# Kernel optimization log

Measured on AMD Instinct MI355X. Metric: run time of the kernel, lower is better.

## Reference

```python
import jax, jax.numpy as jnp
import numpy as np

N_NODES = 20000
N_EDGES = 160000
F_IN = 128
H1 = 1024  # 128 * out_channels
H2 = 512   # 64 * out_channels
OUT = 8    # out_channels


def graph_conv(x, src, dst, w_rel, b_rel, w_root):
    # PyG GraphConv(aggr='mean'): out = lin_rel(mean_{j->i} x_j) + lin_root(x_i)
    n = x.shape[0]
    agg = jax.ops.segment_sum(x[src], dst, num_segments=n)          # [N, F_in]
    deg = jax.ops.segment_sum(jnp.ones((src.shape[0],), x.dtype), dst, num_segments=n)
    mean = agg / jnp.maximum(deg, 1.0)[:, None]
    return mean @ w_rel + b_rel + x @ w_root


def setup_inputs() -> dict:
    key = jax.random.key(0)
    ks = jax.random.split(key, 12)
    x = jax.random.normal(ks[0], (N_NODES, F_IN), dtype=jnp.float32)
    edge_index = jax.random.randint(ks[1], (2, N_EDGES), 0, N_NODES, dtype=jnp.int64)

    def lin(k, fi, fo):
        return jax.random.normal(k, (fi, fo), dtype=jnp.float32) / np.sqrt(fi)

    return {
        "x": x,
        "edge_index": edge_index,
        "w1_rel": lin(ks[2], F_IN, H1), "b1": jnp.zeros((H1,), jnp.float32), "w1_root": lin(ks[3], F_IN, H1),
        "w2_rel": lin(ks[4], H1, H2), "b2": jnp.zeros((H2,), jnp.float32), "w2_root": lin(ks[5], H1, H2),
        "wmu_rel": lin(ks[6], H2, OUT), "bmu": jnp.zeros((OUT,), jnp.float32), "wmu_root": lin(ks[7], H2, OUT),
        "wls_rel": lin(ks[8], H2, OUT), "bls": jnp.zeros((OUT,), jnp.float32), "wls_root": lin(ks[9], H2, OUT),
    }


def reference(x, edge_index, w1_rel, b1, w1_root, w2_rel, b2, w2_root,
              wmu_rel, bmu, wmu_root, wls_rel, bls, wls_root):
    src, dst = edge_index[0], edge_index[1]
    h = jax.nn.relu(graph_conv(x, src, dst, w1_rel, b1, w1_root))
    h = jax.nn.relu(graph_conv(h, src, dst, w2_rel, b2, w2_root))
    mu = graph_conv(h, src, dst, wmu_rel, bmu, wmu_root)
    logstd = graph_conv(h, src, dst, wls_rel, bls, wls_root)
    return (mu, logstd)
```

## Files before the change

### kernel.cpp

```cpp
#include <hip/hip_runtime.h>

typedef __attribute__((ext_vector_type(8))) short short8;
typedef __attribute__((ext_vector_type(4))) float f32x4;
typedef unsigned long long u64;

__device__ __forceinline__ unsigned short f2bf(float f) {
  union { float f; unsigned u; } v; v.f = f;
  unsigned u = v.u;
  unsigned r = (u + 0x7FFFu + ((u >> 16) & 1u)) >> 16;
  return (unsigned short)r;
}
__device__ __forceinline__ float bf2f(unsigned short s) {
  union { unsigned u; float f; } v; v.u = ((unsigned)s) << 16;
  return v.f;
}

__device__ __forceinline__ void gl_lds16(const unsigned short* g, unsigned short* l) {
  __builtin_amdgcn_global_load_lds(
      (const __attribute__((address_space(1))) void*)g,
      (__attribute__((address_space(3))) void*)l, 16, 0, 0);
}

__device__ __forceinline__ int detect64(const void* edges, int n_nodes) {
  const long long* p = (const long long*)edges;
  int ok = 1;
#pragma unroll
  for (int i = 0; i < 8; ++i) {
    long long v = p[i];
    if (v < 0 || v >= n_nodes) ok = 0;
  }
  return ok;
}


__device__ __forceinline__ void ttile(const float* __restrict__ src, int Nw,
                                      unsigned short* __restrict__ dst, int ldd,
                                      int rowoff, int coloff,
                                      int tileIdx, int tilesN, float (*tile)[33]) {
  int tk = tileIdx / tilesN, tn = tileIdx % tilesN;
  int k0 = tk * 32, n0 = tn * 32;
  int tx = threadIdx.x & 31, ty = threadIdx.x >> 5;
#pragma unroll
  for (int s = 0; s < 4; ++s)
    tile[ty + s * 8][tx] = src[(size_t)(k0 + ty + s * 8) * Nw + n0 + tx];
  __syncthreads();
#pragma unroll
  for (int s = 0; s < 4; ++s)
    dst[(size_t)(rowoff + n0 + ty + s * 8) * ldd + coloff + k0 + tx] =
        f2bf(tile[tx][ty + s * 8]);
}

__global__ void prep_kernel(int* deg, int* cursor, int n,
                            const float* __restrict__ x, unsigned short* __restrict__ xb,
                            int total4,
                            const float* __restrict__ w1_rel, const float* __restrict__ w1_root,
                            const float* __restrict__ w2_rel, const float* __restrict__ w2_root,
                            const float* __restrict__ wmu_rel, const float* __restrict__ wmu_root,
                            const float* __restrict__ wls_rel, const float* __restrict__ wls_root,
                            unsigned short* __restrict__ Bt1,
                            unsigned short* __restrict__ Bt2,
                            unsigned short* __restrict__ Bt3) {
  __shared__ float tile[32][33];
  int b = blockIdx.x;
  if (b >= 1408) {
    int b4 = (b - 1408) * 1024;
#pragma unroll
    for (int s = 0; s < 4; ++s) {
      int i4 = b4 + s * 256 + threadIdx.x;
      if (i4 < total4) {
        float4 v = reinterpret_cast<const float4*>(x)[i4];
        ushort4 o;
        o.x = f2bf(v.x); o.y = f2bf(v.y); o.z = f2bf(v.z); o.w = f2bf(v.w);
        reinterpret_cast<ushort4*>(xb)[i4] = o;
      }
    }
    return;
  }
  if (b >= 1344) {
    int i = (b - 1344) * blockDim.x + threadIdx.x;
    int stride = 64 * blockDim.x;
    for (int j = i; j < n; j += stride) { deg[j] = 0; cursor[j] = 0; }
    return;
  }
  if (b < 128)       ttile(w1_rel, 1024, Bt1, 256, 0, 0, b, 32, tile);
  else if (b < 256)  ttile(w1_root, 1024, Bt1, 256, 0, 128, b - 128, 32, tile);
  else if (b < 768)  ttile(w2_rel, 512, Bt2, 1024, 0, 0, b - 256, 16, tile);
  else if (b < 1280) ttile(w2_root, 512, Bt2, 1024, 512, 0, b - 768, 16, tile);
  else {
    int idx = (b - 1280) * 256 + threadIdx.x;
    int nn = idx >> 9, k = idx & 511;
    float v;
    if (nn < 8) v = wmu_rel[(size_t)k * 8 + nn];
    else if (nn < 16) v = wmu_root[(size_t)k * 8 + (nn - 8)];
    else if (nn < 24) v = wls_rel[(size_t)k * 8 + (nn - 16)];
    else v = wls_root[(size_t)k * 8 + (nn - 24)];
    Bt3[(size_t)nn * 512 + k] = f2bf(v);
  }
}

__device__ __forceinline__ int edge_at(const void* p, int is64, size_t idx) {
  return is64 ? (int)((const long long*)p)[idx] : ((const int*)p)[idx];
}

__global__ void count_kernel(const void* edges, int E, int n_nodes, int* deg) {
  int is64 = detect64(edges, n_nodes);
  int i = blockIdx.x * blockDim.x + threadIdx.x;
  int stride = gridDim.x * blockDim.x;
  for (int e = i; e < E; e += stride) {
    int d = edge_at(edges, is64, (size_t)E + e);
    atomicAdd(&deg[d], 1);
  }
}

__global__ void scan_kernel(const int* __restrict__ deg, int* __restrict__ rs,
                            float* __restrict__ invdeg, int n) {
  __shared__ int ssum[1024];
  int tid = threadIdx.x;
  int chunk = (n + 1023) >> 10;
  int start = tid * chunk;
  int end = min(start + chunk, n);
  int s = 0;
  for (int i = start; i < end; ++i) s += deg[i];
  ssum[tid] = s;
  __syncthreads();
  for (int off = 1; off < 1024; off <<= 1) {
    int t = (tid >= off) ? ssum[tid - off] : 0;
    __syncthreads();
    ssum[tid] += t;
    __syncthreads();
  }
  int run = (tid ? ssum[tid - 1] : 0);
  if (tid == 0) rs[0] = 0;
  for (int i = start; i < end; ++i) {
    int d = deg[i];
    run += d;
    rs[i + 1] = run;
    invdeg[i] = 1.0f / fmaxf((float)d, 1.0f);
  }
}

__global__ void fill_kernel(const void* edges, int E, int n_nodes,
                            const int* __restrict__ rs, int* cursor, int* col_src) {
  int is64 = detect64(edges, n_nodes);
  int i = blockIdx.x * blockDim.x + threadIdx.x;
  int stride = gridDim.x * blockDim.x;
  for (int e = i; e < E; e += stride) {
    int d = edge_at(edges, is64, (size_t)E + e);
    int s = edge_at(edges, is64, (size_t)e);
    int p = atomicAdd(&cursor[d], 1);
    col_src[rs[d] + p] = s;
  }
}


__global__ void agg1_kernel(const unsigned short* __restrict__ xb,
                            const int* __restrict__ rs, const int* __restrict__ cs,
                            const float* __restrict__ invdeg,
                            unsigned short* __restrict__ A1, int M) {
  int node = blockIdx.x * 4 + (threadIdx.x >> 6);
  if (node >= M) return;
  int c0 = (threadIdx.x & 63) * 2;
  float a0 = 0.f, a1 = 0.f;
  int e1 = rs[node + 1];
  for (int e = rs[node]; e < e1; ++e) {
    unsigned w = *reinterpret_cast<const unsigned*>(xb + (size_t)cs[e] * 128 + c0);
    a0 += bf2f((unsigned short)(w & 0xffff));
    a1 += bf2f((unsigned short)(w >> 16));
  }
  float inv = invdeg[node];
  unsigned root = *reinterpret_cast<const unsigned*>(xb + (size_t)node * 128 + c0);
  unsigned mean = (unsigned)f2bf(a0 * inv) | ((unsigned)f2bf(a1 * inv) << 16);
  *reinterpret_cast<unsigned*>(A1 + (size_t)node * 256 + c0) = mean;
  *reinterpret_cast<unsigned*>(A1 + (size_t)node * 256 + 128 + c0) = root;
}

__global__ void agg2_kernel(const unsigned short* __restrict__ P2,
                            const int* __restrict__ rs, const int* __restrict__ cs,
                            const float* __restrict__ invdeg,
                            const float* __restrict__ b2,
                            unsigned short* __restrict__ h2, int M) {
  int node = blockIdx.x * 4 + (threadIdx.x >> 6);
  if (node >= M) return;
  int f0 = (threadIdx.x & 63) * 8;
  float acc[8];
#pragma unroll
  for (int v = 0; v < 8; ++v) acc[v] = 0.f;
  int e1 = rs[node + 1];
  for (int e = rs[node]; e < e1; ++e) {
    int s = cs[e];
    uint4 w = *reinterpret_cast<const uint4*>(P2 + (size_t)s * 1024 + f0);
    acc[0] += bf2f((unsigned short)(w.x & 0xffff));
    acc[1] += bf2f((unsigned short)(w.x >> 16));
    acc[2] += bf2f((unsigned short)(w.y & 0xffff));
    acc[3] += bf2f((unsigned short)(w.y >> 16));
    acc[4] += bf2f((unsigned short)(w.z & 0xffff));
    acc[5] += bf2f((unsigned short)(w.z >> 16));
    acc[6] += bf2f((unsigned short)(w.w & 0xffff));
    acc[7] += bf2f((unsigned short)(w.w >> 16));
  }
  float inv = invdeg[node];
  uint4 wr = *reinterpret_cast<const uint4*>(P2 + (size_t)node * 1024 + 512 + f0);
  float rt[8] = {
    bf2f((unsigned short)(wr.x & 0xffff)), bf2f((unsigned short)(wr.x >> 16)),
    bf2f((unsigned short)(wr.y & 0xffff)), bf2f((unsigned short)(wr.y >> 16)),
    bf2f((unsigned short)(wr.z & 0xffff)), bf2f((unsigned short)(wr.z >> 16)),
    bf2f((unsigned short)(wr.w & 0xffff)), bf2f((unsigned short)(wr.w >> 16))};
  unsigned short o[8];
#pragma unroll
  for (int v = 0; v < 8; ++v)
    o[v] = f2bf(fmaxf(acc[v] * inv + rt[v] + b2[f0 + v], 0.f));
  uint4 pk;
  pk.x = (unsigned)o[0] | ((unsigned)o[1] << 16);
  pk.y = (unsigned)o[2] | ((unsigned)o[3] << 16);
  pk.z = (unsigned)o[4] | ((unsigned)o[5] << 16);
  pk.w = (unsigned)o[6] | ((unsigned)o[7] << 16);
  *reinterpret_cast<uint4*>(h2 + (size_t)node * 512 + f0) = pk;
}

__global__ void head_agg_kernel(const float* __restrict__ P3,
                                const int* __restrict__ rs, const int* __restrict__ cs,
                                const float* __restrict__ invdeg,
                                const float* __restrict__ bmu, const float* __restrict__ bls,
                                float* __restrict__ outmu, float* __restrict__ outls, int M) {
  int idx = blockIdx.x * blockDim.x + threadIdx.x;
  int node = idx >> 4;
  int c = idx & 15;
  if (node >= M) return;
  int relc = (c < 8) ? c : (16 + (c - 8));
  float acc = 0.f;
  int e1 = rs[node + 1];
  for (int e = rs[node]; e < e1; ++e) acc += P3[(size_t)cs[e] * 32 + relc];
  float v = acc * invdeg[node] + P3[(size_t)node * 32 + relc + 8]
          + ((c < 8) ? bmu[c] : bls[c - 8]);
  if (c < 8) outmu[(size_t)node * 8 + c] = v;
  else outls[(size_t)node * 8 + (c - 8)] = v;
}

__launch_bounds__(256, 4)
__global__ void gemm_db_kernel(const unsigned short* __restrict__ A, int lda,
                               const unsigned short* __restrict__ Bt, int ldb,
                               const float* __restrict__ bias,
                               void* __restrict__ outp, int ldo,
                               int M, int N, int K, int relu, int out_f32, int gx) {
  __shared__ unsigned short As[2 * 4096];
  __shared__ unsigned short Bs[2 * 4096];
  const int tid = threadIdx.x;
  const int lane = tid & 63;
  const int w = tid >> 6;
  const int wr = w >> 1, wc = w & 1;
  const int lr = lane & 15, lk = lane >> 4;
  const int sw8 = (lk ^ ((lr >> 1) & 3)) * 8;

  int nwg = gridDim.x, orig = blockIdx.x;
  int q = nwg >> 3, r = nwg & 7;
  int xcd = orig & 7, lid = orig >> 3;
  int swz = (xcd < r ? xcd * (q + 1) : r * (q + 1) + (xcd - r) * q) + lid;
  int m0 = (swz / gx) * 128, n0 = (swz % gx) * 128;

  f32x4 acc[4][4];
#pragma unroll
  for (int i = 0; i < 4; ++i)
#pragma unroll
    for (int j = 0; j < 4; ++j) acc[i][j] = (f32x4)0.0f;

  const int r0 = tid >> 2;
  const int slog = ((tid & 3) ^ ((r0 >> 1) & 3)) * 8;
  const unsigned short* gA = A + (size_t)(m0 + r0) * lda + slog;
  const unsigned short* gB = Bt + (size_t)(n0 + r0) * ldb + slog;
  const size_t a64 = (size_t)64 * lda, b64 = (size_t)64 * ldb;
  unsigned short* wa = As + w * 512;
  unsigned short* wb = Bs + w * 512;

  auto STG = [&](int s, int t) {
    const unsigned short* a = gA + (size_t)t * 32;
    const unsigned short* b = gB + (size_t)t * 32;
    gl_lds16(a, wa + s * 4096);
    gl_lds16(a + a64, wa + s * 4096 + 2048);
    gl_lds16(b, wb + s * 4096);
    gl_lds16(b + b64, wb + s * 4096 + 2048);
  };

  const int nt = K >> 5;
  STG(0, 0);
  __syncthreads();

  int buf = 0;
  for (int t = 0; t < nt; ++t) {
    if (t + 1 < nt) STG(buf ^ 1, t + 1);
    const unsigned short* as_ = As + buf * 4096;
    const unsigned short* bs_ = Bs + buf * 4096;
    short8 af[4], bf[4];
#pragma unroll
    for (int i = 0; i < 4; ++i) {
      af[i] = *reinterpret_cast<const short8*>(&as_[(wr * 64 + i * 16 + lr) * 32 + sw8]);
      bf[i] = *reinterpret_cast<const short8*>(&bs_[(wc * 64 + i * 16 + lr) * 32 + sw8]);
    }
    __builtin_amdgcn_s_setprio(1);
#pragma unroll
    for (int i = 0; i < 4; ++i)
#pragma unroll
      for (int j = 0; j < 4; ++j)
        acc[i][j] = __builtin_amdgcn_mfma_f32_16x16x32_bf16(af[i], bf[j], acc[i][j], 0, 0, 0);
    __builtin_amdgcn_s_setprio(0);
    if (t + 1 < nt) __syncthreads();
    buf ^= 1;
  }

#pragma unroll
  for (int i = 0; i < 4; ++i) {
    int row_b = m0 + wr * 64 + i * 16 + lk * 4;
#pragma unroll
    for (int j = 0; j < 4; ++j) {
      int col = n0 + wc * 64 + j * 16 + lr;
      float bv = bias ? bias[col] : 0.f;
#pragma unroll
      for (int rr = 0; rr < 4; ++rr) {
        int row = row_b + rr;
        if (row < M) {
          float v = acc[i][j][rr] + bv;
          if (relu) v = fmaxf(v, 0.f);
          if (out_f32) ((float*)outp)[(size_t)row * ldo + col] = v;
          else ((unsigned short*)outp)[(size_t)row * ldo + col] = f2bf(v);
        }
      }
    }
  }
}

__launch_bounds__(256, 3)
__global__ void gemm_heads_kernel(const unsigned short* __restrict__ A,
                                  const unsigned short* __restrict__ Bt3,
                                  float* __restrict__ P3, int M) {
  __shared__ unsigned short Bs[16 * 1024];
  __shared__ unsigned short As[2 * 4096];
  const int tid = threadIdx.x;
  const int lane = tid & 63;
  const int w = tid >> 6;
  const int lr = lane & 15, lk = lane >> 4;
  const int sw8 = (lk ^ ((lr >> 1) & 3)) * 8;

  int nwg = gridDim.x, orig = blockIdx.x;
  int q = nwg >> 3, r = nwg & 7;
  int xcd = orig & 7, lid = orig >> 3;
  int swz = (xcd < r ? xcd * (q + 1) : r * (q + 1) + (xcd - r) * q) + lid;
  int m0 = swz * 128;

  for (int i = 0; i < 8; ++i) {
    int j = i * 256 + tid;
    int n = j >> 6, p = j & 63;
    int x = (n >> 1) & 3;
    uint4 v = *reinterpret_cast<const uint4*>(Bt3 + (size_t)n * 512 + ((p & ~3) | ((p & 3) ^ x)) * 8);
    *reinterpret_cast<uint4*>(&Bs[(p >> 2) * 1024 + n * 32 + (p & 3) * 8]) = v;
  }

  f32x4 acc[2][2];
#pragma unroll
  for (int i = 0; i < 2; ++i)
#pragma unroll
    for (int j = 0; j < 2; ++j) acc[i][j] = (f32x4)0.0f;

  const int r0 = tid >> 2;
  const int slog = ((tid & 3) ^ ((r0 >> 1) & 3)) * 8;
  const unsigned short* gA = A + (size_t)(m0 + r0) * 512 + slog;
  const size_t a64 = (size_t)64 * 512;
  unsigned short* wa = As + w * 512;

  auto STG = [&](int s, int t) {
    const unsigned short* a = gA + (size_t)t * 32;
    gl_lds16(a, wa + s * 4096);
    gl_lds16(a + a64, wa + s * 4096 + 2048);
  };

  STG(0, 0);
  __syncthreads();

  int buf = 0;
  const int nt = 16;
  for (int t = 0; t < nt; ++t) {
    if (t + 1 < nt) STG(buf ^ 1, t + 1);
    const unsigned short* as_ = As + buf * 4096;
    short8 af[2], bf[2];
#pragma unroll
    for (int i = 0; i < 2; ++i) {
      af[i] = *reinterpret_cast<const short8*>(&as_[(w * 32 + i * 16 + lr) * 32 + sw8]);
      bf[i] = *reinterpret_cast<const short8*>(&Bs[t * 1024 + (i * 16 + lr) * 32 + sw8]);
    }
#pragma unroll
    for (int i = 0; i < 2; ++i)
#pragma unroll
      for (int j = 0; j < 2; ++j)
        acc[i][j] = __builtin_amdgcn_mfma_f32_16x16x32_bf16(af[i], bf[j], acc[i][j], 0, 0, 0);
    if (t + 1 < nt) __syncthreads();
    buf ^= 1;
  }

#pragma unroll
  for (int i = 0; i < 2; ++i) {
    int row_b = m0 + w * 32 + i * 16 + lk * 4;
#pragma unroll
    for (int j = 0; j < 2; ++j) {
      int col = j * 16 + lr;
#pragma unroll
      for (int rr = 0; rr < 4; ++rr) {
        int row = row_b + rr;
        if (row < M) P3[(size_t)row * 32 + col] = acc[i][j][rr];
      }
    }
  }
}


extern "C" void kernel_launch(void* const* d_in, const int* in_sizes, int n_in,
                              void* d_out, int out_size, void* d_ws, size_t ws_size,
                              hipStream_t stream) {
  const float* x = (const float*)d_in[0];
  const void* edge = d_in[1];
  const float* w1_rel = (const float*)d_in[2];
  const float* b1 = (const float*)d_in[3];
  const float* w1_root = (const float*)d_in[4];
  const float* w2_rel = (const float*)d_in[5];
  const float* b2 = (const float*)d_in[6];
  const float* w2_root = (const float*)d_in[7];
  const float* wmu_rel = (const float*)d_in[8];
  const float* bmu = (const float*)d_in[9];
  const float* wmu_root = (const float*)d_in[10];
  const float* wls_rel = (const float*)d_in[11];
  const float* bls = (const float*)d_in[12];
  const float* wls_root = (const float*)d_in[13];

  const int FIN = 128, H1 = 1024, H2 = 512;
  const int M = in_sizes[0] / FIN;
  const int E = in_sizes[1] / 2;
  const int Mpad = ((M + 127) / 128) * 128;
  const int gy = Mpad / 128;

  char* ws = (char*)d_ws;
  size_t off = 0;
  auto alloc = [&](size_t bytes) -> char* {
    char* p = ws + off;
    off = (off + bytes + 255) & ~(size_t)255;
    return p;
  };
  int* deg = (int*)alloc((size_t)M * 4);
  int* cursor = (int*)alloc((size_t)M * 4);
  int* rs = (int*)alloc((size_t)(M + 1) * 4);
  float* invdeg = (float*)alloc((size_t)M * 4);
  int* cs = (int*)alloc((size_t)E * 4);
  unsigned short* xb = (unsigned short*)alloc((size_t)M * 128 * 2);
  unsigned short* A1 = (unsigned short*)alloc((size_t)Mpad * 256 * 2);
  unsigned short* h1 = (unsigned short*)alloc((size_t)Mpad * 1024 * 2);
  unsigned short* P2 = (unsigned short*)alloc((size_t)Mpad * 1024 * 2);
  unsigned short* h2 = (unsigned short*)alloc((size_t)Mpad * 512 * 2);
  float* P3 = (float*)alloc((size_t)Mpad * 32 * 4);
  unsigned short* Bt1 = (unsigned short*)alloc((size_t)H1 * 256 * 2);
  unsigned short* Bt2 = (unsigned short*)alloc((size_t)1024 * 1024 * 2);
  unsigned short* Bt3 = (unsigned short*)alloc((size_t)32 * 512 * 2);

  prep_kernel<<<2048, 256, 0, stream>>>(deg, cursor, M,
                                        x, xb, M * FIN / 4,
                                        w1_rel, w1_root, w2_rel, w2_root,
                                        wmu_rel, wmu_root, wls_rel, wls_root,
                                        Bt1, Bt2, Bt3);
  count_kernel<<<256, 256, 0, stream>>>(edge, E, M, deg);
  scan_kernel<<<1, 1024, 0, stream>>>(deg, rs, invdeg, M);
  fill_kernel<<<256, 256, 0, stream>>>(edge, E, M, rs, cursor, cs);

  agg1_kernel<<<(M + 3) / 4, 256, 0, stream>>>(xb, rs, cs, invdeg, A1, M);
  gemm_db_kernel<<<(H1 / 128) * gy, 256, 0, stream>>>(
      A1, 256, Bt1, 256, b1, h1, 1024, M, H1, 256, 1, 0, H1 / 128);

  gemm_db_kernel<<<(1024 / 128) * gy, 256, 0, stream>>>(
      h1, 1024, Bt2, 1024, nullptr, P2, 1024, M, 1024, 1024, 0, 0, 1024 / 128);
  agg2_kernel<<<(M + 3) / 4, 256, 0, stream>>>(P2, rs, cs, invdeg, b2, h2, M);

  gemm_heads_kernel<<<gy, 256, 0, stream>>>(h2, Bt3, P3, M);
  float* outmu = (float*)d_out;
  float* outls = outmu + (size_t)M * 8;
  head_agg_kernel<<<(M * 16 + 255) / 256, 256, 0, stream>>>(
      P3, rs, cs, invdeg, bmu, bls, outmu, outls, M);
}
```

Measured before the change: 236.8 us.

## Fuse CSR build into one cooperative kernel with grid-wide syncs

Replaces the separate count, single-block scan and fill kernels, plus the degree/cursor zeroing in prep, with one cooperative kernel of 512 blocks that uses grid.sync between phases. The scan becomes a multi-block scan: each block scans locally and then sums earlier block totals read from a small buffer. This removes several kernel launches and spreads the serial 1024-thread scan across the whole GPU. It adds four grid-wide barriers and relies on all 512 blocks being co-resident for the cooperative launch.

```diff
diff --git a/kernel.cpp b/kernel.cpp
--- a/kernel.cpp
+++ b/kernel.cpp
@@ -1,4 +1,7 @@
 #include <hip/hip_runtime.h>
+#include <hip/hip_cooperative_groups.h>
+
+namespace cg = cooperative_groups;
 
 typedef __attribute__((ext_vector_type(8))) short short8;
 typedef __attribute__((ext_vector_type(4))) float f32x4;
@@ -30,6 +33,10 @@
     if (v < 0 || v >= n_nodes) ok = 0;
   }
   return ok;
+}
+
+__device__ __forceinline__ int edge_at(const void* p, int is64, size_t idx) {
+  return is64 ? (int)((const long long*)p)[idx] : ((const int*)p)[idx];
 }
 
 
@@ -50,8 +57,7 @@
         f2bf(tile[tx][ty + s * 8]);
 }
 
-__global__ void prep_kernel(int* deg, int* cursor, int n,
-                            const float* __restrict__ x, unsigned short* __restrict__ xb,
+__global__ void prep_kernel(const float* __restrict__ x, unsigned short* __restrict__ xb,
                             int total4,
                             const float* __restrict__ w1_rel, const float* __restrict__ w1_root,
                             const float* __restrict__ w2_rel, const float* __restrict__ w2_root,
@@ -62,8 +68,8 @@
                             unsigned short* __restrict__ Bt3) {
   __shared__ float tile[32][33];
   int b = blockIdx.x;
-  if (b >= 1408) {
-    int b4 = (b - 1408) * 1024;
+  if (b >= 1344) {
+    int b4 = (b - 1344) * 1024;
 #pragma unroll
     for (int s = 0; s < 4; ++s) {
       int i4 = b4 + s * 256 + threadIdx.x;
@@ -74,12 +80,6 @@
         reinterpret_cast<ushort4*>(xb)[i4] = o;
       }
     }
-    return;
-  }
-  if (b >= 1344) {
-    int i = (b - 1344) * blockDim.x + threadIdx.x;
-    int stride = 64 * blockDim.x;
-    for (int j = i; j < n; j += stride) { deg[j] = 0; cursor[j] = 0; }
     return;
   }
   if (b < 128)       ttile(w1_rel, 1024, Bt1, 256, 0, 0, b, 32, tile);
@@ -98,57 +98,61 @@
   }
 }
 
-__device__ __forceinline__ int edge_at(const void* p, int is64, size_t idx) {
-  return is64 ? (int)((const long long*)p)[idx] : ((const int*)p)[idx];
-}
-
-__global__ void count_kernel(const void* edges, int E, int n_nodes, int* deg) {
-  int is64 = detect64(edges, n_nodes);
-  int i = blockIdx.x * blockDim.x + threadIdx.x;
-  int stride = gridDim.x * blockDim.x;
-  for (int e = i; e < E; e += stride) {
+__global__ void csr_kernel(const void* edges, int E, int M,
+                           int* deg, int* cursor, int* rs, float* invdeg,
+                           int* cs, int* bsum) {
+  cg::grid_group grid = cg::this_grid();
+  __shared__ int s[256];
+  const int t = threadIdx.x;
+  const int b = blockIdx.x;
+  const int gid = b * 256 + t;
+  const int nthreads = gridDim.x * 256;
+  const int is64 = detect64(edges, M);
+
+  for (int i = gid; i < M; i += nthreads) { deg[i] = 0; cursor[i] = 0; }
+  grid.sync();
+
+  for (int e = gid; e < E; e += nthreads) {
     int d = edge_at(edges, is64, (size_t)E + e);
     atomicAdd(&deg[d], 1);
   }
-}
-
-__global__ void scan_kernel(const int* __restrict__ deg, int* __restrict__ rs,
-                            float* __restrict__ invdeg, int n) {
-  __shared__ int ssum[1024];
-  int tid = threadIdx.x;
-  int chunk = (n + 1023) >> 10;
-  int start = tid * chunk;
-  int end = min(start + chunk, n);
-  int s = 0;
-  for (int i = start; i < end; ++i) s += deg[i];
-  ssum[tid] = s;
+  grid.sync();
+
+  const int chunk = (M + nthreads - 1) / nthreads;
+  const int start = gid * chunk;
+  const int end = min(start + chunk, M);
+  int local = 0;
+  for (int i = start; i < end; ++i) local += deg[i];
+  s[t] = local;
   __syncthreads();
-  for (int off = 1; off < 1024; off <<= 1) {
-    int t = (tid >= off) ? ssum[tid - off] : 0;
+  for (int off = 1; off < 256; off <<= 1) {
+    int tv = (t >= off) ? s[t - off] : 0;
     __syncthreads();
-    ssum[tid] += t;
+    s[t] += tv;
     __syncthreads();
   }
-  int run = (tid ? ssum[tid - 1] : 0);
-  if (tid == 0) rs[0] = 0;
+  if (t == 255) bsum[b] = s[255];
+  grid.sync();
+  int boff = 0;
+  for (int i = 0; i < (int)gridDim.x; ++i) {
+    int v = bsum[i];
+    if (i < b) boff += v;
+  }
+  int run = boff + s[t] - local;
+  if (gid == 0) rs[0] = 0;
   for (int i = start; i < end; ++i) {
     int d = deg[i];
     run += d;
     rs[i + 1] = run;
     invdeg[i] = 1.0f / fmaxf((float)d, 1.0f);
   }
-}
-
-__global__ void fill_kernel(const void* edges, int E, int n_nodes,
-                            const int* __restrict__ rs, int* cursor, int* col_src) {
-  int is64 = detect64(edges, n_nodes);
-  int i = blockIdx.x * blockDim.x + threadIdx.x;
-  int stride = gridDim.x * blockDim.x;
-  for (int e = i; e < E; e += stride) {
+  grid.sync();
+
+  for (int e = gid; e < E; e += nthreads) {
     int d = edge_at(edges, is64, (size_t)E + e);
-    int s = edge_at(edges, is64, (size_t)e);
+    int sv = edge_at(edges, is64, (size_t)e);
     int p = atomicAdd(&cursor[d], 1);
-    col_src[rs[d] + p] = s;
+    cs[rs[d] + p] = sv;
   }
 }
 
@@ -446,6 +450,7 @@
   int* rs = (int*)alloc((size_t)(M + 1) * 4);
   float* invdeg = (float*)alloc((size_t)M * 4);
   int* cs = (int*)alloc((size_t)E * 4);
+  int* bsum = (int*)alloc(512 * 4);
   unsigned short* xb = (unsigned short*)alloc((size_t)M * 128 * 2);
   unsigned short* A1 = (unsigned short*)alloc((size_t)Mpad * 256 * 2);
   unsigned short* h1 = (unsigned short*)alloc((size_t)Mpad * 1024 * 2);
@@ -456,14 +461,16 @@
   unsigned short* Bt2 = (unsigned short*)alloc((size_t)1024 * 1024 * 2);
   unsigned short* Bt3 = (unsigned short*)alloc((size_t)32 * 512 * 2);
 
-  prep_kernel<<<2048, 256, 0, stream>>>(deg, cursor, M,
-                                        x, xb, M * FIN / 4,
+  prep_kernel<<<1984, 256, 0, stream>>>(x, xb, M * FIN / 4,
                                         w1_rel, w1_root, w2_rel, w2_root,
                                         wmu_rel, wmu_root, wls_rel, wls_root,
                                         Bt1, Bt2, Bt3);
-  count_kernel<<<256, 256, 0, stream>>>(edge, E, M, deg);
-  scan_kernel<<<1, 1024, 0, stream>>>(deg, rs, invdeg, M);
-  fill_kernel<<<256, 256, 0, stream>>>(edge, E, M, rs, cursor, cs);
+
+  {
+    void* args[] = {(void*)&edge, (void*)&E, (void*)&M, (void*)&deg, (void*)&cursor,
+                    (void*)&rs, (void*)&invdeg, (void*)&cs, (void*)&bsum};
+    hipLaunchCooperativeKernel((void*)csr_kernel, dim3(512), dim3(256), args, 0, stream);
+  }
 
   agg1_kernel<<<(M + 3) / 4, 256, 0, stream>>>(xb, rs, cs, invdeg, A1, M);
   gemm_db_kernel<<<(H1 / 128) * gy, 256, 0, stream>>>(
```

Measured after the change: 458.8 us. 93.7% more time.
